# Kernel tuning notes

Measured on AMD Instinct MI355X. Metric: run time of the kernel, lower is better.

## Reference

```python
import jax, jax.numpy as jnp
import numpy as np

POOL_K = 8        # predictor_kernel_size
THRESH = 0.05     # predictor_threshold
EPS = 1e-5        # masked_fill value


def _round_ste(x):
    # straight-through round (forward: round)
    return x + jax.lax.stop_gradient(jnp.round(x) - x)


def _quant_act_uint(x, scale, bits):
    # Brevitas Uint8ActPerTensorFloat-style fake quant: unsigned, per-tensor scale
    n = 2.0 ** bits - 1.0
    return jnp.clip(_round_ste(x / scale), 0.0, n) * scale


def _quant_weight_per_oc(w, bits):
    # signed, narrow-range, per-output-channel scaling: s = max|w| / (2^(b-1)-1)
    n = 2.0 ** (bits - 1) - 1.0
    s = jnp.max(jnp.abs(w), axis=(1, 2, 3), keepdims=True) / n
    return jnp.clip(_round_ste(w / s), -n, n) * s


def _conv(x, w):
    return jax.lax.conv_general_dilated(
        x, w, window_strides=(1, 1), padding=((1, 1), (1, 1)),
        dimension_numbers=('NCHW', 'OIHW', 'NCHW'))


def _predictor_mask(x):
    # AvgPool2d(8) (stride=kernel) -> threshold -> nearest upsample back to HxW
    B, C, H, W = x.shape
    pooled = x.reshape(B, C, H // POOL_K, POOL_K, W // POOL_K, POOL_K).mean(axis=(3, 5))
    m = pooled >= THRESH
    m = jnp.repeat(jnp.repeat(m, POOL_K, axis=2), POOL_K, axis=3)  # nearest interp
    return jax.lax.stop_gradient(m)  # mask.detach()


def setup_inputs() -> dict:
    key = jax.random.key(0)
    k1, k2, k3 = jax.random.split(key, 3)
    x = jax.random.normal(k1, (32, 128, 56, 56), jnp.float32)
    w_high = jax.random.normal(k2, (128, 128, 3, 3), jnp.float32) * 0.05
    w_low = jax.random.normal(k3, (128, 128, 3, 3), jnp.float32) * 0.05
    return {
        'x': x,
        'w_high': w_high,
        'w_low': w_low,
        'act_scale_high': jnp.float32(0.02),
        'act_scale_low': jnp.float32(0.04),
    }


def reference(x, w_high, w_low, act_scale_high, act_scale_low):
    mask = _predictor_mask(x)                 # [B,C,H,W] bool
    x_high = jnp.where(mask, x, EPS)          # masked_fill(~mask, 1e-5)
    x_low = jnp.where(mask, EPS, x)           # masked_fill(mask, 1e-5)
    y_high = _conv(_quant_act_uint(x_high, act_scale_high, 8),
                   _quant_weight_per_oc(w_high, 8))
    y_low = _conv(_quant_act_uint(x_low, act_scale_low, 4),
                  _quant_weight_per_oc(w_low, 4))
    return y_high + y_low
```

## Files before the change

### kernel.cpp

```cpp
#include <hip/hip_runtime.h>
#include <hip/hip_bf16.h>
#include <stdint.h>

#define BATCH 32
#define CH 128
#define HH 56
#define WW 56
#define HW 3136
#define M_TOTAL (BATCH*HW)
#define PLANE ((size_t)M_TOTAL * 16)

using int4v   = __attribute__((ext_vector_type(4))) int;
using float4v = __attribute__((ext_vector_type(4))) float;

#define WQB_OFF 0
#define SCB_OFF 294912
#define ZP_OFF  296448
#define AQN_OFF 296704

#define GLD_LDS16(g, l)                                                        \
  __builtin_amdgcn_global_load_lds(                                            \
      (const __attribute__((address_space(1))) void*)(g),                      \
      (__attribute__((address_space(3))) void*)(l), 16, 0, 0)

#define KSTR 484

__global__ __launch_bounds__(256) void prep_kernel(
    const float* __restrict__ x,
    const float* __restrict__ wh, const float* __restrict__ wl,
    const float* __restrict__ p_sh, const float* __restrict__ p_sl,
    char* __restrict__ wqb, float* __restrict__ scb, int* __restrict__ zp,
    char* __restrict__ aqn) {
  __shared__ __align__(16) float smem[16 * KSTR + 128];
  int t = threadIdx.x;

  if (blockIdx.x >= BATCH * 7 * 8) {
    int blk = blockIdx.x - BATCH * 7 * 8;
    int which = blk >> 7, oc = blk & 127;
    if (blk == 0 && t < 64)
      zp[t] = (t < 32) ? 0x80808080 : 0;
    const float* src = (which ? wl : wh) + (size_t)oc * 1152;
    float n = which ? 7.0f : 127.0f;
    float* red = smem;
    int* ired = (int*)(smem + 256);

    float m = 0.0f;
    for (int e = t; e < 1152; e += 256) m = fmaxf(m, fabsf(src[e]));
    red[t] = m;
    __syncthreads();
    for (int s = 128; s > 0; s >>= 1) {
      if (t < s) red[t] = fmaxf(red[t], red[t + s]);
      __syncthreads();
    }
    float scale = red[0] / n;

    int partial = 0;
    for (int e = t; e < 1152; e += 256) {
      int tt = e >> 7, ic = e & 127;
      float q = rintf(src[ic * 9 + tt] / scale);
      q = fminf(fmaxf(q, -n), n);
      int k = (int)q;
      partial += k;
      wqb[((size_t)tt * 128 + oc) * 256 + which * 128 + ic] = (char)k;
    }
    ired[t] = partial;
    __syncthreads();
    for (int s = 128; s > 0; s >>= 1) {
      if (t < s) ired[t] += ired[t + s];
      __syncthreads();
    }
    if (t == 0) {
      float s_act = which ? p_sl[0] : p_sh[0];
      float sc = s_act * scale;
      if (which == 0) {
        scb[oc] = sc;
        scb[256 + oc] = sc * 128.0f * (float)ired[0];
      } else {
        scb[128 + oc] = sc;
      }
    }
    return;
  }

  int bi = blockIdx.x;
  int cg = bi & 7;
  int bb = bi >> 3;
  int b = bb / 7, band = bb - b * 7;
  float* sx = smem;
  float* smk = smem + 16 * KSTR;
  #pragma unroll
  for (int i = 0; i < 7; ++i) {
    int idx = i * 256 + t;
    int k = idx / 112, rem = idx - k * 112;
    int r = rem / 14, w4 = rem - r * 14;
    *(float4v*)(sx + k * KSTR + r * 60 + w4 * 4) =
        *(const float4v*)(x + ((size_t)(b * 128 + cg * 16 + k)) * HW
                            + (band * 8 + r) * 56 + w4 * 4);
  }
  __syncthreads();
  if (t < 112) {
    int k = t / 7, bw = t - (t / 7) * 7;
    float s = 0.0f;
    #pragma unroll
    for (int r = 0; r < 8; ++r)
      #pragma unroll
      for (int j = 0; j < 8; ++j)
        s += sx[k * KSTR + r * 60 + bw * 8 + j];
    smk[t] = (s * (1.0f / 64.0f) >= 0.05f) ? 1.0f : 0.0f;
  }
  __syncthreads();
  float shs = p_sh[0], sls = p_sl[0];
  #pragma unroll
  for (int it = 0; it < 2; ++it) {
    int pos = it * 256 + t;
    if (pos < 448) {
      int r = pos / 56, w = pos - r * 56;
      int h = band * 8 + r;
      size_t gp = (size_t)b * HW + (size_t)h * 56 + w;
      int hw_[4] = {0, 0, 0, 0}, lw_[4] = {0, 0, 0, 0};
      int mcell = w >> 3;
      #pragma unroll
      for (int k = 0; k < 16; ++k) {
        float xv = sx[k * KSTR + r * 60 + w];
        bool mk = smk[k * 7 + mcell] != 0.0f;
        float xh = mk ? xv : 1e-5f;
        int kh = (int)fminf(fmaxf(rintf(xh / shs), 0.0f), 255.0f) - 128;
        float xl = mk ? 1e-5f : xv;
        int kl = (int)fminf(fmaxf(rintf(xl / sls), 0.0f), 15.0f);
        hw_[k >> 2] |= (kh & 0xff) << ((k & 3) * 8);
        lw_[k >> 2] |= (kl & 0xff) << ((k & 3) * 8);
      }
      *(int4v*)(aqn + ((size_t)cg * M_TOTAL + gp) * 16) =
          (int4v){hw_[0], hw_[1], hw_[2], hw_[3]};
      *(int4v*)(aqn + ((size_t)(8 + cg) * M_TOTAL + gp) * 16) =
          (int4v){lw_[0], lw_[1], lw_[2], lw_[3]};
    }
  }
}

__global__ __launch_bounds__(256, 3) void conv_mfma_kernel(
    const char* __restrict__ wqb,
    const char* __restrict__ aqn,
    const char* __restrict__ zp,
    const float* __restrict__ scb,
    float* __restrict__ out) {
  __shared__ __align__(16) char As[2][160 * 64];
  __shared__ __align__(16) char Bs[2][192 * 64];

  int tid = threadIdx.x;
  int lane = tid & 63, wv = tid >> 6;
  int wm = wv >> 1, wn = wv & 1;
  int lr = lane & 15, quad = lane >> 4;
  int bx = blockIdx.x;
  int m0 = (((bx & 7) * 98) + (bx >> 3)) * 128;
  int oc0 = blockIdx.y * 64;

  int ng = (wv < 2) ? 3 : 2;
  int sgrp[3] = {wv, wv + 4, wv + 8};
  const char* abase[3];
  const char* zbase[3];
  int avalid[3], ah[3];
  #pragma unroll
  for (int j = 0; j < 3; ++j) {
    int slot = sgrp[j] * 16 + (lane >> 2);
    int q = ((lane & 3) ^ (slot >> 1)) & 3;
    int p = m0 + slot - 16;
    int pv = (p >= 0) && (p < M_TOTAL);
    int pc = pv ? p : 0;
    int bb = pc / HW, rem = pc - bb * HW;
    int hh = rem / 56;
    abase[j] = aqn + (size_t)q * PLANE + (size_t)pc * 16;
    zbase[j] = zp + q * 16;
    avalid[j] = pv;
    ah[j] = hh;
  }
  const char* bbase[3];
  #pragma unroll
  for (int i = 0; i < 3; ++i) {
    int slot = wv * 48 + i * 16 + (lane >> 2);
    int qp = (((lane & 3) ^ (slot >> 1)) & 3) * 16;
    int dwi_s = slot >> 6, ocr = slot & 63;
    bbase[i] = wqb + ((size_t)(dwi_s * 128 + oc0 + ocr)) * 256 + qp;
  }
  int lo_ok[4], hi_ok[4];
  #pragma unroll
  for (int mi = 0; mi < 4; ++mi) {
    int m = m0 + wm * 64 + mi * 16 + lr;
    int w = (m % HW) % 56;
    lo_ok[mi] = (w > 0);
    hi_ok[mi] = (w < 55);
  }

  int4v acch[4][2], accl[4][2];
  #pragma unroll
  for (int mi = 0; mi < 4; ++mi)
    #pragma unroll
    for (int ni = 0; ni < 2; ++ni) {
      acch[mi][ni] = (int4v){0, 0, 0, 0};
      accl[mi][ni] = (int4v){0, 0, 0, 0};
    }

  auto stage = [&](int s, char* A, char* B) {
    int dh3 = s >> 2, icc = s & 3;
    int dh = dh3 - 1;
    #pragma unroll
    for (int j = 0; j < 3; ++j) {
      if (j < ng) {
        int h2 = ah[j] + dh;
        bool ok = avalid[j] && ((unsigned)h2 < (unsigned)HH);
        const char* p = ok ? (abase[j] + dh * (56 * 16) + (size_t)icc * (4 * PLANE))
                           : (zbase[j] + icc * 64);
        GLD_LDS16(p, A + sgrp[j] * 1024);
      }
    }
    #pragma unroll
    for (int i = 0; i < 3; ++i)
      GLD_LDS16(bbase[i] + (size_t)dh3 * 98304 + icc * 64,
                B + (wv * 48 + i * 16) * 64);
  };

  auto compute = [&](int s, const char* A, const char* B) {
    int icc = s & 3;
    const bool high = (icc < 2);
    const int patv = high ? (int)0x80808080 : 0;
    const int4v pat = (int4v){patv, patv, patv, patv};
    #pragma unroll
    for (int dwi = 0; dwi < 3; ++dwi) {
      int4v af[4], bf[2];
      #pragma unroll
      for (int mi = 0; mi < 4; ++mi) {
        int sA = wm * 64 + mi * 16 + lr + 15 + dwi;
        af[mi] = *(const int4v*)(A + sA * 64 + (((quad ^ (sA >> 1)) & 3) * 16));
        bool ok = (dwi == 1) | (dwi == 0 ? lo_ok[mi] : hi_ok[mi]);
        af[mi] = ok ? af[mi] : pat;
      }
      #pragma unroll
      for (int ni = 0; ni < 2; ++ni) {
        int sB = dwi * 64 + wn * 32 + ni * 16 + lr;
        bf[ni] = *(const int4v*)(B + sB * 64 + (((quad ^ (sB >> 1)) & 3) * 16));
      }
      __builtin_amdgcn_s_setprio(1);
      if (high) {
        #pragma unroll
        for (int mi = 0; mi < 4; ++mi)
          #pragma unroll
          for (int ni = 0; ni < 2; ++ni)
            acch[mi][ni] = __builtin_amdgcn_mfma_i32_16x16x64_i8(
                af[mi], bf[ni], acch[mi][ni], 0, 0, 0);
      } else {
        #pragma unroll
        for (int mi = 0; mi < 4; ++mi)
          #pragma unroll
          for (int ni = 0; ni < 2; ++ni)
            accl[mi][ni] = __builtin_amdgcn_mfma_i32_16x16x64_i8(
                af[mi], bf[ni], accl[mi][ni], 0, 0, 0);
      }
      __builtin_amdgcn_s_setprio(0);
    }
  };

  stage(0, As[0], Bs[0]);
  __syncthreads();
  #pragma unroll
  for (int s = 0; s < 12; ++s) {
    if (s < 11) stage(s + 1, As[(s + 1) & 1], Bs[(s + 1) & 1]);
    compute(s, As[s & 1], Bs[s & 1]);
    __syncthreads();
  }

  #pragma unroll
  for (int mi = 0; mi < 4; ++mi) {
    int m = m0 + wm * 64 + mi * 16 + quad * 4;
    int b = m / HW, r = m - b * HW;
    float* obase = out + (size_t)b * (CH * HW) + r;
    #pragma unroll
    for (int ni = 0; ni < 2; ++ni) {
      int oc = oc0 + wn * 32 + ni * 16 + lr;
      float sch = scb[oc], scl = scb[128 + oc], bs = scb[256 + oc];
      float4v f;
      #pragma unroll
      for (int rg = 0; rg < 4; ++rg)
        f[rg] = sch * (float)acch[mi][ni][rg] + scl * (float)accl[mi][ni][rg] + bs;
      __builtin_nontemporal_store(f, (float4v*)(obase + (size_t)oc * HW));
    }
  }
}

extern "C" void kernel_launch(void* const* d_in, const int* in_sizes, int n_in,
                              void* d_out, int out_size, void* d_ws, size_t ws_size,
                              hipStream_t stream) {
  const float* x  = (const float*)d_in[0];
  const float* wh = (const float*)d_in[1];
  const float* wl = (const float*)d_in[2];
  const float* sh = (const float*)d_in[3];
  const float* sl = (const float*)d_in[4];
  float* out = (float*)d_out;

  char* ws = (char*)d_ws;
  char* wqb  = ws + WQB_OFF;
  float* scb = (float*)(ws + SCB_OFF);
  int* zp    = (int*)(ws + ZP_OFF);
  char* aqn  = ws + AQN_OFF;

  prep_kernel<<<dim3(BATCH * 7 * 8 + 256), dim3(256), 0, stream>>>(
      x, wh, wl, sh, sl, wqb, scb, zp, aqn);
  conv_mfma_kernel<<<dim3(M_TOTAL / 128, 2), dim3(256), 0, stream>>>(
      wqb, aqn, (const char*)zp, scb, out);
}
```

Baseline: 157.7 us.

## Load weight fragments directly into registers and shrink the A halo in LDS

Weight (B) tiles are no longer staged through LDS. Each lane now loads its MFMA B fragments straight from global memory into a double-buffered register array, one stage ahead. The A tile halo is reduced from 16 to 8 rows (144 slots), which cuts LDS footprint and the number of global-to-LDS loads per stage. The aim is to lower LDS traffic and usage, possibly raising occupancy. The cost is more VGPRs and redundant global or L2 reads of weights, since both wm waves fetch the same B fragments.

```diff
diff --git a/kernel.cpp b/kernel.cpp
--- a/kernel.cpp
+++ b/kernel.cpp
@@ -144,8 +144,7 @@
     const char* __restrict__ zp,
     const float* __restrict__ scb,
     float* __restrict__ out) {
-  __shared__ __align__(16) char As[2][160 * 64];
-  __shared__ __align__(16) char Bs[2][192 * 64];
+  __shared__ __align__(16) char As[2][144 * 64];
 
   int tid = threadIdx.x;
   int lane = tid & 63, wv = tid >> 6;
@@ -155,7 +154,7 @@
   int m0 = (((bx & 7) * 98) + (bx >> 3)) * 128;
   int oc0 = blockIdx.y * 64;
 
-  int ng = (wv < 2) ? 3 : 2;
+  int ng = (wv == 0) ? 3 : 2;
   int sgrp[3] = {wv, wv + 4, wv + 8};
   const char* abase[3];
   const char* zbase[3];
@@ -164,7 +163,7 @@
   for (int j = 0; j < 3; ++j) {
     int slot = sgrp[j] * 16 + (lane >> 2);
     int q = ((lane & 3) ^ (slot >> 1)) & 3;
-    int p = m0 + slot - 16;
+    int p = m0 + slot - 8;
     int pv = (p >= 0) && (p < M_TOTAL);
     int pc = pv ? p : 0;
     int bb = pc / HW, rem = pc - bb * HW;
@@ -174,14 +173,8 @@
     avalid[j] = pv;
     ah[j] = hh;
   }
-  const char* bbase[3];
-  #pragma unroll
-  for (int i = 0; i < 3; ++i) {
-    int slot = wv * 48 + i * 16 + (lane >> 2);
-    int qp = (((lane & 3) ^ (slot >> 1)) & 3) * 16;
-    int dwi_s = slot >> 6, ocr = slot & 63;
-    bbase[i] = wqb + ((size_t)(dwi_s * 128 + oc0 + ocr)) * 256 + qp;
-  }
+  const char* bq = wqb + ((size_t)(oc0 + wn * 32 + lr)) * 256 + quad * 16;
+
   int lo_ok[4], hi_ok[4];
   #pragma unroll
   for (int mi = 0; mi < 4; ++mi) {
@@ -200,7 +193,7 @@
       accl[mi][ni] = (int4v){0, 0, 0, 0};
     }
 
-  auto stage = [&](int s, char* A, char* B) {
+  auto stageA = [&](int s, char* A) {
     int dh3 = s >> 2, icc = s & 3;
     int dh = dh3 - 1;
     #pragma unroll
@@ -213,31 +206,31 @@
         GLD_LDS16(p, A + sgrp[j] * 1024);
       }
     }
-    #pragma unroll
-    for (int i = 0; i < 3; ++i)
-      GLD_LDS16(bbase[i] + (size_t)dh3 * 98304 + icc * 64,
-                B + (wv * 48 + i * 16) * 64);
   };
-
-  auto compute = [&](int s, const char* A, const char* B) {
+  auto loadB = [&](int s, int4v (&bf)[6]) {
+    int dh3 = s >> 2, icc = s & 3;
+    #pragma unroll
+    for (int dwi = 0; dwi < 3; ++dwi)
+      #pragma unroll
+      for (int ni = 0; ni < 2; ++ni)
+        bf[dwi * 2 + ni] = *(const int4v*)(
+            bq + (size_t)(((dh3 * 3 + dwi) * 128 + ni * 16)) * 256 + icc * 64);
+  };
+
+  auto compute = [&](int s, const char* A, const int4v (&bf6)[6]) {
     int icc = s & 3;
     const bool high = (icc < 2);
     const int patv = high ? (int)0x80808080 : 0;
     const int4v pat = (int4v){patv, patv, patv, patv};
     #pragma unroll
     for (int dwi = 0; dwi < 3; ++dwi) {
-      int4v af[4], bf[2];
+      int4v af[4];
       #pragma unroll
       for (int mi = 0; mi < 4; ++mi) {
-        int sA = wm * 64 + mi * 16 + lr + 15 + dwi;
+        int sA = wm * 64 + mi * 16 + lr + 7 + dwi;
         af[mi] = *(const int4v*)(A + sA * 64 + (((quad ^ (sA >> 1)) & 3) * 16));
         bool ok = (dwi == 1) | (dwi == 0 ? lo_ok[mi] : hi_ok[mi]);
         af[mi] = ok ? af[mi] : pat;
-      }
-      #pragma unroll
-      for (int ni = 0; ni < 2; ++ni) {
-        int sB = dwi * 64 + wn * 32 + ni * 16 + lr;
-        bf[ni] = *(const int4v*)(B + sB * 64 + (((quad ^ (sB >> 1)) & 3) * 16));
       }
       __builtin_amdgcn_s_setprio(1);
       if (high) {
@@ -246,25 +239,30 @@
           #pragma unroll
           for (int ni = 0; ni < 2; ++ni)
             acch[mi][ni] = __builtin_amdgcn_mfma_i32_16x16x64_i8(
-                af[mi], bf[ni], acch[mi][ni], 0, 0, 0);
+                af[mi], bf6[dwi * 2 + ni], acch[mi][ni], 0, 0, 0);
       } else {
         #pragma unroll
         for (int mi = 0; mi < 4; ++mi)
           #pragma unroll
           for (int ni = 0; ni < 2; ++ni)
             accl[mi][ni] = __builtin_amdgcn_mfma_i32_16x16x64_i8(
-                af[mi], bf[ni], accl[mi][ni], 0, 0, 0);
+                af[mi], bf6[dwi * 2 + ni], accl[mi][ni], 0, 0, 0);
       }
       __builtin_amdgcn_s_setprio(0);
     }
   };
 
-  stage(0, As[0], Bs[0]);
+  int4v bfr[2][6];
+  stageA(0, As[0]);
+  loadB(0, bfr[0]);
   __syncthreads();
   #pragma unroll
   for (int s = 0; s < 12; ++s) {
-    if (s < 11) stage(s + 1, As[(s + 1) & 1], Bs[(s + 1) & 1]);
-    compute(s, As[s & 1], Bs[s & 1]);
+    if (s < 11) {
+      loadB(s + 1, bfr[(s + 1) & 1]);
+      stageA(s + 1, As[(s + 1) & 1]);
+    }
+    compute(s, As[s & 1], bfr[s & 1]);
     __syncthreads();
   }
 
```

After: 192.5 us. 22.0% more time.

## Use two waves per block with 64x64 per-wave tiles in conv kernel

Applied to the files above, without the earlier changes.

Shrinks the conv block from four waves to two. Each wave now computes all 64 output channels for its 64 rows, which doubles accumulators and B-fragment reuse per wave. The A/B staging loads are redistributed across the two waves, and B is issued before A. The output store switches from nontemporal to a regular store. Register pressure rises (32 int4 accumulators), and fewer threads per block means fewer waves to hide latency.

```diff
diff --git a/kernel.cpp b/kernel.cpp
--- a/kernel.cpp
+++ b/kernel.cpp
@@ -138,7 +138,7 @@
   }
 }
 
-__global__ __launch_bounds__(256, 3) void conv_mfma_kernel(
+__global__ __launch_bounds__(128, 2) void conv_mfma_kernel(
     const char* __restrict__ wqb,
     const char* __restrict__ aqn,
     const char* __restrict__ zp,
@@ -149,19 +149,18 @@
 
   int tid = threadIdx.x;
   int lane = tid & 63, wv = tid >> 6;
-  int wm = wv >> 1, wn = wv & 1;
   int lr = lane & 15, quad = lane >> 4;
   int bx = blockIdx.x;
   int m0 = (((bx & 7) * 98) + (bx >> 3)) * 128;
   int oc0 = blockIdx.y * 64;
 
-  int ng = (wv < 2) ? 3 : 2;
-  int sgrp[3] = {wv, wv + 4, wv + 8};
-  const char* abase[3];
-  const char* zbase[3];
-  int avalid[3], ah[3];
-  #pragma unroll
-  for (int j = 0; j < 3; ++j) {
+  int sgrp[5];
+  const char* abase[5];
+  const char* zbase[5];
+  int avalid[5], ah[5];
+  #pragma unroll
+  for (int j = 0; j < 5; ++j) {
+    sgrp[j] = wv + 2 * j;
     int slot = sgrp[j] * 16 + (lane >> 2);
     int q = ((lane & 3) ^ (slot >> 1)) & 3;
     int p = m0 + slot - 16;
@@ -174,10 +173,10 @@
     avalid[j] = pv;
     ah[j] = hh;
   }
-  const char* bbase[3];
-  #pragma unroll
-  for (int i = 0; i < 3; ++i) {
-    int slot = wv * 48 + i * 16 + (lane >> 2);
+  const char* bbase[6];
+  #pragma unroll
+  for (int i = 0; i < 6; ++i) {
+    int slot = (wv * 6 + i) * 16 + (lane >> 2);
     int qp = (((lane & 3) ^ (slot >> 1)) & 3) * 16;
     int dwi_s = slot >> 6, ocr = slot & 63;
     bbase[i] = wqb + ((size_t)(dwi_s * 128 + oc0 + ocr)) * 256 + qp;
@@ -185,38 +184,39 @@
   int lo_ok[4], hi_ok[4];
   #pragma unroll
   for (int mi = 0; mi < 4; ++mi) {
-    int m = m0 + wm * 64 + mi * 16 + lr;
+    int m = m0 + wv * 64 + mi * 16 + lr;
     int w = (m % HW) % 56;
     lo_ok[mi] = (w > 0);
     hi_ok[mi] = (w < 55);
   }
 
-  int4v acch[4][2], accl[4][2];
+  int4v acch[4][4], accl[4][4];
   #pragma unroll
   for (int mi = 0; mi < 4; ++mi)
     #pragma unroll
-    for (int ni = 0; ni < 2; ++ni) {
+    for (int ni = 0; ni < 4; ++ni) {
       acch[mi][ni] = (int4v){0, 0, 0, 0};
       accl[mi][ni] = (int4v){0, 0, 0, 0};
     }
 
-  auto stage = [&](int s, char* A, char* B) {
+  auto stageA = [&](int s, char* A) {
     int dh3 = s >> 2, icc = s & 3;
     int dh = dh3 - 1;
     #pragma unroll
-    for (int j = 0; j < 3; ++j) {
-      if (j < ng) {
-        int h2 = ah[j] + dh;
-        bool ok = avalid[j] && ((unsigned)h2 < (unsigned)HH);
-        const char* p = ok ? (abase[j] + dh * (56 * 16) + (size_t)icc * (4 * PLANE))
-                           : (zbase[j] + icc * 64);
-        GLD_LDS16(p, A + sgrp[j] * 1024);
-      }
-    }
-    #pragma unroll
-    for (int i = 0; i < 3; ++i)
+    for (int j = 0; j < 5; ++j) {
+      int h2 = ah[j] + dh;
+      bool ok = avalid[j] && ((unsigned)h2 < (unsigned)HH);
+      const char* p = ok ? (abase[j] + dh * (56 * 16) + (size_t)icc * (4 * PLANE))
+                         : (zbase[j] + icc * 64);
+      GLD_LDS16(p, A + sgrp[j] * 1024);
+    }
+  };
+  auto stageB = [&](int s, char* B) {
+    int dh3 = s >> 2, icc = s & 3;
+    #pragma unroll
+    for (int i = 0; i < 6; ++i)
       GLD_LDS16(bbase[i] + (size_t)dh3 * 98304 + icc * 64,
-                B + (wv * 48 + i * 16) * 64);
+                B + ((wv * 6 + i) * 16) * 64);
   };
 
   auto compute = [&](int s, const char* A, const char* B) {
@@ -226,17 +226,17 @@
     const int4v pat = (int4v){patv, patv, patv, patv};
     #pragma unroll
     for (int dwi = 0; dwi < 3; ++dwi) {
-      int4v af[4], bf[2];
+      int4v af[4], bf[4];
       #pragma unroll
       for (int mi = 0; mi < 4; ++mi) {
-        int sA = wm * 64 + mi * 16 + lr + 15 + dwi;
+        int sA = wv * 64 + mi * 16 + lr + 15 + dwi;
         af[mi] = *(const int4v*)(A + sA * 64 + (((quad ^ (sA >> 1)) & 3) * 16));
         bool ok = (dwi == 1) | (dwi == 0 ? lo_ok[mi] : hi_ok[mi]);
         af[mi] = ok ? af[mi] : pat;
       }
       #pragma unroll
-      for (int ni = 0; ni < 2; ++ni) {
-        int sB = dwi * 64 + wn * 32 + ni * 16 + lr;
+      for (int ni = 0; ni < 4; ++ni) {
+        int sB = dwi * 64 + ni * 16 + lr;
         bf[ni] = *(const int4v*)(B + sB * 64 + (((quad ^ (sB >> 1)) & 3) * 16));
       }
       __builtin_amdgcn_s_setprio(1);
@@ -244,14 +244,14 @@
         #pragma unroll
         for (int mi = 0; mi < 4; ++mi)
           #pragma unroll
-          for (int ni = 0; ni < 2; ++ni)
+          for (int ni = 0; ni < 4; ++ni)
             acch[mi][ni] = __builtin_amdgcn_mfma_i32_16x16x64_i8(
                 af[mi], bf[ni], acch[mi][ni], 0, 0, 0);
       } else {
         #pragma unroll
         for (int mi = 0; mi < 4; ++mi)
           #pragma unroll
-          for (int ni = 0; ni < 2; ++ni)
+          for (int ni = 0; ni < 4; ++ni)
             accl[mi][ni] = __builtin_amdgcn_mfma_i32_16x16x64_i8(
                 af[mi], bf[ni], accl[mi][ni], 0, 0, 0);
       }
@@ -259,29 +259,33 @@
     }
   };
 
-  stage(0, As[0], Bs[0]);
+  stageA(0, As[0]);
+  stageB(0, Bs[0]);
   __syncthreads();
   #pragma unroll
   for (int s = 0; s < 12; ++s) {
-    if (s < 11) stage(s + 1, As[(s + 1) & 1], Bs[(s + 1) & 1]);
+    if (s < 11) {
+      stageB(s + 1, Bs[(s + 1) & 1]);
+      stageA(s + 1, As[(s + 1) & 1]);
+    }
     compute(s, As[s & 1], Bs[s & 1]);
     __syncthreads();
   }
 
   #pragma unroll
   for (int mi = 0; mi < 4; ++mi) {
-    int m = m0 + wm * 64 + mi * 16 + quad * 4;
+    int m = m0 + wv * 64 + mi * 16 + quad * 4;
     int b = m / HW, r = m - b * HW;
     float* obase = out + (size_t)b * (CH * HW) + r;
     #pragma unroll
-    for (int ni = 0; ni < 2; ++ni) {
-      int oc = oc0 + wn * 32 + ni * 16 + lr;
+    for (int ni = 0; ni < 4; ++ni) {
+      int oc = oc0 + ni * 16 + lr;
       float sch = scb[oc], scl = scb[128 + oc], bs = scb[256 + oc];
       float4v f;
       #pragma unroll
       for (int rg = 0; rg < 4; ++rg)
         f[rg] = sch * (float)acch[mi][ni][rg] + scl * (float)accl[mi][ni][rg] + bs;
-      __builtin_nontemporal_store(f, (float4v*)(obase + (size_t)oc * HW));
+      *(float4v*)(obase + (size_t)oc * HW) = f;
     }
   }
 }
@@ -304,6 +308,6 @@
 
   prep_kernel<<<dim3(BATCH * 7 * 8 + 256), dim3(256), 0, stream>>>(
       x, wh, wl, sh, sl, wqb, scb, zp, aqn);
-  conv_mfma_kernel<<<dim3(M_TOTAL / 128, 2), dim3(256), 0, stream>>>(
+  conv_mfma_kernel<<<dim3(M_TOTAL / 128, 2), dim3(128), 0, stream>>>(
       wqb, aqn, (const char*)zp, scb, out);
 }
```

Result: slower. 164.4 us (+4.2%).
